# Kernel tuning notes

Measured on AMD Instinct MI355X. Metric: run time of the kernel, lower is better.

Reference implementation:

```python
import jax, jax.numpy as jnp
import numpy as np

N_HEAD = 16
D_MODEL = 1024
D_K = D_MODEL // N_HEAD  # 64
NEG = -1000000000.0


def setup_inputs() -> dict:
    key = jax.random.key(0)
    ks = jax.random.split(key, 7)
    B, L = 4, 2048
    q = jax.random.normal(ks[0], (B, L, D_MODEL), dtype=jnp.float32)
    k = jax.random.normal(ks[1], (B, L, D_MODEL), dtype=jnp.float32)
    v = jax.random.normal(ks[2], (B, L, D_MODEL), dtype=jnp.float32)
    mask = jnp.ones((B, L, L), dtype=jnp.int32)
    s = 1.0 / np.sqrt(D_MODEL)
    w_q = jax.random.normal(ks[3], (D_MODEL, D_MODEL), dtype=jnp.float32) * s
    w_k = jax.random.normal(ks[4], (D_MODEL, D_MODEL), dtype=jnp.float32) * s
    w_v = jax.random.normal(ks[5], (D_MODEL, D_MODEL), dtype=jnp.float32) * s
    w_o = jax.random.normal(ks[6], (D_MODEL, D_MODEL), dtype=jnp.float32) * s
    return {"q": q, "k": k, "v": v, "w_q": w_q, "w_k": w_k, "w_v": w_v, "w_o": w_o, "mask": mask}


def reference(q, k, v, w_q, w_k, w_v, w_o, mask):
    B, Lq, _ = q.shape
    temperature = jnp.asarray(D_K, q.dtype) ** 0.5
    # Projections (Linear, no bias): x @ W^T, then split heads -> [B, H, L, d_k]
    qh = (q @ w_q.T).reshape(B, Lq, N_HEAD, D_K).transpose(0, 2, 1, 3)
    kh = (k @ w_k.T).reshape(B, -1, N_HEAD, D_K).transpose(0, 2, 1, 3)
    vh = (v @ w_v.T).reshape(B, -1, N_HEAD, D_K).transpose(0, 2, 1, 3)
    # Scaled dot-product attention, full [B, H, Lq, Lk] scores materialized
    attn = jnp.einsum("bhqd,bhkd->bhqk", qh / temperature, kh)
    attn = jnp.where(mask[:, None, :, :] == 0, NEG, attn)
    attn = jax.nn.softmax(attn, axis=-1)  # dropout is identity in eval mode
    out = jnp.einsum("bhqk,bhkd->bhqd", attn, vh)
    out = out.transpose(0, 2, 1, 3).reshape(B, Lq, D_MODEL)
    return out @ w_o.T
```

## Files before the change

### kernel.cpp

```cpp
#include <hip/hip_runtime.h>
#include <stdint.h>

typedef float  f32x4  __attribute__((ext_vector_type(4)));
typedef __bf16 bf16x8 __attribute__((ext_vector_type(8)));
typedef short  s16x8  __attribute__((ext_vector_type(8)));
typedef short  s16x4  __attribute__((ext_vector_type(4)));
typedef unsigned int   u32;
typedef unsigned short u16;
typedef u32 u32x2 __attribute__((ext_vector_type(2)));
typedef u32 u32x4 __attribute__((ext_vector_type(4)));

#define DM 1024
#define LQ 2048
#define NH 16

__device__ __forceinline__ u16 f2bf(float f) {
    unsigned int u = __builtin_bit_cast(unsigned int, f);
    u += 0x7FFFu + ((u >> 16) & 1u);
    return (u16)(u >> 16);
}

__device__ __forceinline__ float fexp2(float x) {
#if __has_builtin(__builtin_amdgcn_exp2f)
    return __builtin_amdgcn_exp2f(x);
#else
    return exp2f(x);
#endif
}

__device__ __forceinline__ u32 cvtpk(float lo, float hi) {
    u32 r;
    asm("v_cvt_pk_bf16_f32 %0, %1, %2" : "=v"(r) : "v"(lo), "v"(hi));
    return r;
}

__device__ __forceinline__ float max3f(float a, float b, float c) {
    float r;
    asm("v_max3_f32 %0, %1, %2, %3" : "=v"(r) : "v"(a), "v"(b), "v"(c));
    return r;
}

__device__ __forceinline__ u32 permb(u32 b, u32 a, u32 sel) {
    u32 r;
    asm("v_perm_b32 %0, %1, %2, %3" : "=v"(r) : "v"(b), "v"(a), "s"(sel));
    return r;
}

__device__ __forceinline__ f32x4 mfma32(s16x8 a, s16x8 b, f32x4 c) {
    return __builtin_amdgcn_mfma_f32_16x16x32_bf16(
        __builtin_bit_cast(bf16x8, a), __builtin_bit_cast(bf16x8, b), c, 0, 0, 0);
}

#define GLD16(gp, lp) __builtin_amdgcn_global_load_lds( \
    (__attribute__((address_space(1))) void*)(gp),      \
    (__attribute__((address_space(3))) void*)(lp), 16, 0, 0)

__global__ void k_cvt_mask(const float4* __restrict__ wq, const float4* __restrict__ wk,
                           const float4* __restrict__ wv, const float4* __restrict__ wo,
                           uint64_t* bwq, uint64_t* bwk, uint64_t* bwv, uint64_t* bwo,
                           const int4* __restrict__ m4, int* flag)
{
    const int NW = 262144;
    const int totw = 4 * NW;
    const int totm = (4 * 2048 * 2048) / 4;
    const int stride = gridDim.x * blockDim.x;
    bool z = false;
    for (int idx = blockIdx.x * blockDim.x + threadIdx.x; idx < totw + totm;
         idx += stride) {
        if (idx < totw) {
            int ji = idx >> 18, off = idx & (NW - 1);
            const float4* s = ji == 0 ? wq : ji == 1 ? wk : ji == 2 ? wv : wo;
            uint64_t* d = ji == 0 ? bwq : ji == 1 ? bwk : ji == 2 ? bwv : bwo;
            float4 f = s[off];
            union { u16 u[4]; uint64_t qq; } rr;
            rr.u[0] = f2bf(f.x); rr.u[1] = f2bf(f.y);
            rr.u[2] = f2bf(f.z); rr.u[3] = f2bf(f.w);
            d[off] = rr.qq;
        } else {
            int4 v = m4[idx - totw];
            if (v.x == 0 || v.y == 0 || v.z == 0 || v.w == 0) z = true;
        }
    }
    if (__ballot(z)) {
        if ((threadIdx.x & 63) == 0) atomicAnd(flag, 0);
    }
}

template <int MODE>
__global__ __launch_bounds__(256) void k_gemm(
    const float* __restrict__ Aq, const float* __restrict__ Ak,
    const float* __restrict__ Av, const u16* __restrict__ Ab,
    const u16* __restrict__ Bw0,
    u16* __restrict__ Cb0, float* __restrict__ Cf, float scale)
{
    constexpr int K = 1024;
    __shared__ char lA[128 * 32 * 2];
    __shared__ char lB[128 * 32 * 2];
    const int t = threadIdx.x, l = t & 63, w = t >> 6;
    const int q = l & 15, g = l >> 4;
    const int z = (MODE == 0) ? blockIdx.z : 0;
    const float* Af = (MODE == 0) ? (z == 0 ? Aq : (z == 1 ? Ak : Av)) : nullptr;
    const u16* Bw = Bw0 + (size_t)z * 1048576;
    u16* Cb = (MODE == 0) ? Cb0 + (size_t)z * 8388608 : nullptr;
    const float scl = (MODE == 0 && z != 0) ? 1.0f : scale;
    const int lin = blockIdx.x;
    const int ytile = ((lin & 7) << 3) | ((lin >> 3) & 7);
    const int xtile = lin >> 6;
    const int m0 = ytile * 128, n0 = xtile * 128;
    const int wr = (w >> 1) * 64, wc = (w & 1) * 64;

    f32x4 acc[4][4];
#pragma unroll
    for (int i = 0; i < 4; i++)
#pragma unroll
        for (int j = 0; j < 4; j++) acc[i][j] = (f32x4){0.f, 0.f, 0.f, 0.f};

    for (int k0 = 0; k0 < K; k0 += 32) {
        if (MODE == 0) {
            float4 f0[2], f1[2];
#pragma unroll
            for (int c = 0; c < 2; c++) {
                int i = c * 256 + t;
                int row = i >> 2, sl = i & 3;
                int ss = sl ^ (row & 3);
                const float* ap = Af + (size_t)(m0 + row) * K + k0 + ss * 8;
                f0[c] = *(const float4*)ap;
                f1[c] = *(const float4*)(ap + 4);
            }
#pragma unroll
            for (int c = 0; c < 2; c++) {
                int i = c * 256 + t;
                int row = i >> 2, sl = i & 3;
                int ss = sl ^ (row & 3);
                GLD16(Bw + (size_t)(n0 + row) * K + k0 + ss * 8, lB + (i - l) * 16);
            }
#pragma unroll
            for (int c = 0; c < 2; c++) {
                int i = c * 256 + t;
                u32x4 pk = {cvtpk(f0[c].x, f0[c].y), cvtpk(f0[c].z, f0[c].w),
                            cvtpk(f1[c].x, f1[c].y), cvtpk(f1[c].z, f1[c].w)};
                *(u32x4*)(lA + i * 16) = pk;
            }
        } else {
#pragma unroll
            for (int c = 0; c < 2; c++) {
                int i = c * 256 + t;
                int row = i >> 2, sl = i & 3;
                int ss = sl ^ (row & 3);
                GLD16(Ab + (size_t)(m0 + row) * K + k0 + ss * 8, lA + (i - l) * 16);
                GLD16(Bw + (size_t)(n0 + row) * K + k0 + ss * 8, lB + (i - l) * 16);
            }
        }
        __syncthreads();
        s16x8 af[4], bfr[4];
#pragma unroll
        for (int mt = 0; mt < 4; mt++) {
            int r = wr + mt * 16 + q;
            af[mt] = *(const s16x8*)(lA + r * 64 + ((g ^ (r & 3)) * 16));
        }
#pragma unroll
        for (int nt = 0; nt < 4; nt++) {
            int r = wc + nt * 16 + q;
            bfr[nt] = *(const s16x8*)(lB + r * 64 + ((g ^ (r & 3)) * 16));
        }
#pragma unroll
        for (int mt = 0; mt < 4; mt++)
#pragma unroll
            for (int nt = 0; nt < 4; nt++)
                acc[mt][nt] = mfma32(bfr[nt], af[mt], acc[mt][nt]);
        __syncthreads();
    }

#pragma unroll
    for (int mt = 0; mt < 4; mt++) {
        int m = m0 + wr + mt * 16 + q;
#pragma unroll
        for (int nt = 0; nt < 4; nt++) {
            int n = n0 + wc + nt * 16 + g * 4;
            f32x4 a = acc[mt][nt];
            if (MODE == 0) {
                int bb = m >> 11, row = m & 2047;
                int h = n >> 6, d = n & 63;
                s16x4 pk;
#pragma unroll
                for (int j = 0; j < 4; j++) pk[j] = (short)f2bf(a[j] * scl);
                *(s16x4*)(Cb + (((size_t)(bb * NH + h) * LQ + row) << 6) + d) = pk;
            } else {
                f32x4 o;
#pragma unroll
                for (int j = 0; j < 4; j++) o[j] = a[j] * scl;
                *(f32x4*)(Cf + (size_t)m * DM + n) = o;
            }
        }
    }
}

__global__ __launch_bounds__(256, 2) void k_attn(
    const u16* __restrict__ Qh, const u16* __restrict__ Kh,
    const u16* __restrict__ Vh, u16* __restrict__ ctx,
    const int* __restrict__ mask, const int* __restrict__ flag)
{
    __shared__ char lds[32768];
    char* lK0 = lds;
    char* lV0 = lds + 16384;
    const int t = threadIdx.x, l = t & 63, w = t >> 6;
    const int g = l >> 4, q = l & 15;
    const int p = blockIdx.x;
    const int bh = (p & 7) * 8 + ((p >> 3) >> 3);
    const int qt = ((p >> 3) & 7) * 256;
    const int allones = *flag;
    const size_t base = (size_t)bh * LQ * 64;
    const int dg = (l & 7) | ((w & 2) << 2);
    const int kg = (l >> 3) | ((w & 1) << 3);

    s16x8 qf[4][2];
#pragma unroll
    for (int qh = 0; qh < 4; qh++)
#pragma unroll
        for (int kh = 0; kh < 2; kh++)
            qf[qh][kh] = *(const s16x8*)(
                Qh + base + (size_t)(qt + w * 64 + qh * 16 + q) * 64 + kh * 32 + g * 8);

    f32x4 oacc[4][4];
#pragma unroll
    for (int qh = 0; qh < 4; qh++)
#pragma unroll
        for (int dt = 0; dt < 4; dt++) oacc[qh][dt] = (f32x4){0.f, 0.f, 0.f, 0.f};
    float mrow[4] = {-1e30f, -1e30f, -1e30f, -1e30f};
    float lrow[4] = {0.f, 0.f, 0.f, 0.f};

    auto stageK = [&](int kt, int b) {
#pragma unroll
        for (int c = 0; c < 2; c++) {
            int i = c * 256 + t;
            int row = i >> 3, sl = i & 7;
            GLD16(Kh + base + (size_t)(kt + row) * 64 + ((sl ^ (row & 7)) * 8),
                  lK0 + b * 8192 + (i - l) * 16);
        }
    };
    auto loadV = [&](int kt, s16x4* vr) {
#pragma unroll
        for (int j = 0; j < 4; j++)
            vr[j] = *(const s16x4*)(Vh + base + (size_t)(kt + kg * 4 + j) * 64 + dg * 4);
    };
    auto writeV = [&](const s16x4* vr, int b) {
        const u32 selLO = 0x05040100u, selHI = 0x07060302u;
        const int u = ((kg & 8) >> 1) | (kg & 3);
        const int bb2 = (kg >> 2) & 1;
        u32x2 vv[4];
#pragma unroll
        for (int j = 0; j < 4; j++) vv[j] = __builtin_bit_cast(u32x2, vr[j]);
#pragma unroll
        for (int jj = 0; jj < 4; jj++) {
            int d = dg * 4 + jj;
            u32 a0 = vv[0][jj >> 1], a1 = vv[1][jj >> 1];
            u32 a2 = vv[2][jj >> 1], a3 = vv[3][jj >> 1];
            u32 sel = (jj & 1) ? selHI : selLO;
            u32x2 pw = {permb(a1, a0, sel), permb(a3, a2, sel)};
            *(s16x4*)(lV0 + b * 8192 + d * 128 + ((u ^ (d & 7)) * 16) + bb2 * 8) =
                __builtin_bit_cast(s16x4, pw);
        }
    };

    {
        s16x4 vr[4];
        stageK(0, 0);
        loadV(0, vr);
        writeV(vr, 0);
    }

    int cur = 0;
    for (int kt = 0; kt < LQ; kt += 64) {
        __syncthreads();
        const bool more = (kt + 64) < LQ;
        s16x4 vr[4];
        if (more) {
            stageK(kt + 64, cur ^ 1);
            loadV(kt + 64, vr);
        }

        f32x4 sc[4][4];
#pragma unroll
        for (int qh = 0; qh < 4; qh++)
#pragma unroll
            for (int ct = 0; ct < 4; ct++) sc[qh][ct] = (f32x4){0.f, 0.f, 0.f, 0.f};
        __builtin_amdgcn_s_setprio(1);
#pragma unroll
        for (int ct = 0; ct < 4; ct++) {
            int kc = ct * 16 + q;
#pragma unroll
            for (int kh = 0; kh < 2; kh++) {
                s16x8 kf = *(const s16x8*)(lK0 + cur * 8192 + kc * 128 +
                                           (((kh * 4 + g) ^ (kc & 7)) * 16));
#pragma unroll
                for (int qh = 0; qh < 4; qh++)
                    sc[qh][ct] = mfma32(kf, qf[qh][kh], sc[qh][ct]);
            }
        }
        __builtin_amdgcn_s_setprio(0);

        if (!allones) {
            int b = bh >> 4;
#pragma unroll
            for (int qh = 0; qh < 4; qh++)
#pragma unroll
                for (int ct = 0; ct < 4; ct++)
#pragma unroll
                    for (int r = 0; r < 4; r++) {
                        int qr = qt + w * 64 + qh * 16 + q;
                        int kc = kt + ct * 16 + g * 4 + r;
                        if (mask[(size_t)(b * LQ + qr) * LQ + kc] == 0)
                            sc[qh][ct][r] = -1e9f;
                    }
        }

        float pm[4];
#pragma unroll
        for (int qh = 0; qh < 4; qh++) {
            float m0 = max3f(sc[qh][0][0], sc[qh][0][1], sc[qh][0][2]);
            m0 = max3f(m0, sc[qh][0][3], sc[qh][1][0]);
            m0 = max3f(m0, sc[qh][1][1], sc[qh][1][2]);
            m0 = max3f(m0, sc[qh][1][3], sc[qh][2][0]);
            m0 = max3f(m0, sc[qh][2][1], sc[qh][2][2]);
            m0 = max3f(m0, sc[qh][2][3], sc[qh][3][0]);
            m0 = max3f(m0, sc[qh][3][1], sc[qh][3][2]);
            m0 = fmaxf(m0, sc[qh][3][3]);
            m0 = fmaxf(m0, __shfl_xor(m0, 16, 64));
            m0 = fmaxf(m0, __shfl_xor(m0, 32, 64));
            pm[qh] = m0;
        }
        bool ok = pm[0] <= mrow[0] + 8.f;
        ok = ok && (pm[1] <= mrow[1] + 8.f);
        ok = ok && (pm[2] <= mrow[2] + 8.f);
        ok = ok && (pm[3] <= mrow[3] + 8.f);
        if (!__all(ok)) {
#pragma unroll
            for (int qh = 0; qh < 4; qh++) {
                float nm = fmaxf(mrow[qh], pm[qh]);
                float corr = fexp2(mrow[qh] - nm);
                mrow[qh] = nm;
                lrow[qh] *= corr;
                float cv[4];
#pragma unroll
                for (int r = 0; r < 4; r++) cv[r] = __shfl(corr, g * 4 + r, 64);
#pragma unroll
                for (int dt = 0; dt < 4; dt++)
#pragma unroll
                    for (int r = 0; r < 4; r++) oacc[qh][dt][r] *= cv[r];
            }
        }
        s16x8 pa32[4][2];
#pragma unroll
        for (int qh = 0; qh < 4; qh++) {
#pragma unroll
            for (int ct = 0; ct < 4; ct++)
#pragma unroll
                for (int r = 0; r < 4; r++)
                    sc[qh][ct][r] = fexp2(sc[qh][ct][r] - mrow[qh]);
            f32x4 vs = (sc[qh][0] + sc[qh][1]) + (sc[qh][2] + sc[qh][3]);
            float rs = (vs[0] + vs[1]) + (vs[2] + vs[3]);
            rs += __shfl_xor(rs, 16, 64);
            rs += __shfl_xor(rs, 32, 64);
            lrow[qh] += rs;
#pragma unroll
            for (int s = 0; s < 2; s++) {
                u32x4 pv;
                pv.x = cvtpk(sc[qh][2 * s][0],     sc[qh][2 * s][1]);
                pv.y = cvtpk(sc[qh][2 * s][2],     sc[qh][2 * s][3]);
                pv.z = cvtpk(sc[qh][2 * s + 1][0], sc[qh][2 * s + 1][1]);
                pv.w = cvtpk(sc[qh][2 * s + 1][2], sc[qh][2 * s + 1][3]);
                pa32[qh][s] = __builtin_bit_cast(s16x8, pv);
            }
        }

        __builtin_amdgcn_s_setprio(1);
#pragma unroll
        for (int dt = 0; dt < 4; dt++) {
#pragma unroll
            for (int s = 0; s < 2; s++) {
                s16x8 vf = *(const s16x8*)(lV0 + cur * 8192 + (dt * 16 + q) * 128 +
                                           (((4 * s + g) ^ (q & 7)) * 16));
#pragma unroll
                for (int qh = 0; qh < 4; qh++)
                    oacc[qh][dt] = mfma32(pa32[qh][s], vf, oacc[qh][dt]);
            }
        }
        __builtin_amdgcn_s_setprio(0);

        if (more) writeV(vr, cur ^ 1);
        cur ^= 1;
    }

    __syncthreads();
    char* eb = lds + w * 8192;
#pragma unroll
    for (int qh = 0; qh < 4; qh++) {
        float lv[4];
#pragma unroll
        for (int r = 0; r < 4; r++) lv[r] = 1.f / __shfl(lrow[qh], g * 4 + r, 64);
#pragma unroll
        for (int dt = 0; dt < 4; dt++)
#pragma unroll
            for (int r = 0; r < 4; r++) {
                int row = qh * 16 + g * 4 + r;
                int cb = ((dt * 16 + q) * 2) ^ ((row & 7) << 4);
                *(u16*)(eb + row * 128 + cb) = f2bf(oacc[qh][dt][r] * lv[r]);
            }
    }
    __syncthreads();
    const int b = bh >> 4, h = bh & 15;
    const int token = qt + w * 64 + l;
    u16* gp = ctx + (size_t)(b * LQ + token) * DM + h * 64;
#pragma unroll
    for (int j = 0; j < 8; j++) {
        int cb = (j * 16) ^ ((l & 7) << 4);
        *(s16x8*)(gp + j * 8) = *(const s16x8*)(eb + l * 128 + cb);
    }
}

extern "C" void kernel_launch(void* const* d_in, const int* in_sizes, int n_in,
                              void* d_out, int out_size, void* d_ws, size_t ws_size,
                              hipStream_t stream)
{
    const float* q  = (const float*)d_in[0];
    const float* k  = (const float*)d_in[1];
    const float* v  = (const float*)d_in[2];
    const float* wq = (const float*)d_in[3];
    const float* wk = (const float*)d_in[4];
    const float* wv = (const float*)d_in[5];
    const float* wo = (const float*)d_in[6];
    const int* mask = (const int*)d_in[7];

    char* ws = (char*)d_ws;
    const size_t SX = (size_t)8192 * 1024 * 2;
    const size_t SW = (size_t)1024 * 1024 * 2;
    u16* bwq = (u16*)(ws + 3 * SX);
    u16* bwk = (u16*)(ws + 3 * SX + SW);
    u16* bwv = (u16*)(ws + 3 * SX + 2 * SW);
    u16* bwo = (u16*)(ws + 3 * SX + 3 * SW);
    u16* Qh  = (u16*)(ws + 3 * SX + 4 * SW);
    u16* Kh  = (u16*)(ws + 4 * SX + 4 * SW);
    u16* Vh  = (u16*)(ws + 5 * SX + 4 * SW);
    u16* ctx = (u16*)(ws + 6 * SX + 4 * SW);
    int* flag = (int*)(ws + 7 * SX + 4 * SW);

    hipMemsetAsync(flag, 0xFF, 4, stream);
    k_cvt_mask<<<2048, 256, 0, stream>>>(
        (const float4*)wq, (const float4*)wk, (const float4*)wv, (const float4*)wo,
        (uint64_t*)bwq, (uint64_t*)bwk, (uint64_t*)bwv, (uint64_t*)bwo,
        (const int4*)mask, flag);

    k_gemm<0><<<dim3(512, 1, 3), 256, 0, stream>>>(
        q, k, v, nullptr, bwq, Qh, nullptr, 0.18033688011112042f);

    k_attn<<<512, 256, 0, stream>>>(Qh, Kh, Vh, ctx, mask, flag);

    k_gemm<1><<<dim3(512), 256, 0, stream>>>(
        nullptr, nullptr, nullptr, ctx, bwo, nullptr, (float*)d_out, 1.0f);
}
```

Baseline: 239.7 us.

## Pre-convert activations to bf16 and double-buffer GEMM LDS loads

Adds a separate kernel that converts the q, k and v activations to bf16 in workspace, so the projection GEMM can load A through global_load_lds like the output GEMM. The GEMM now double-buffers its LDS tiles, prefetching the next K-slice during the MFMAs, drops one barrier per iteration, and raises wave priority around the MFMA block. This targets load latency and conversion work inside the GEMM main loop. The cost is an extra pass that reads 96MB of fp32 and writes 48MB of bf16, plus doubled LDS per block.

```diff
diff --git a/kernel.cpp b/kernel.cpp
--- a/kernel.cpp
+++ b/kernel.cpp
@@ -54,6 +54,25 @@
 #define GLD16(gp, lp) __builtin_amdgcn_global_load_lds( \
     (__attribute__((address_space(1))) void*)(gp),      \
     (__attribute__((address_space(3))) void*)(lp), 16, 0, 0)
+
+__global__ void k_cvt_act(const float4* __restrict__ q, const float4* __restrict__ k,
+                          const float4* __restrict__ v,
+                          uint64_t* xq, uint64_t* xk, uint64_t* xv)
+{
+    const int NX = 2097152;
+    const int stride = gridDim.x * blockDim.x;
+    for (int idx = blockIdx.x * blockDim.x + threadIdx.x; idx < 3 * NX;
+         idx += stride) {
+        int ji = idx >> 21, off = idx & (NX - 1);
+        const float4* s = ji == 0 ? q : ji == 1 ? k : v;
+        uint64_t* d = ji == 0 ? xq : ji == 1 ? xk : xv;
+        float4 f = s[off];
+        union { u16 u[4]; uint64_t qq; } rr;
+        rr.u[0] = f2bf(f.x); rr.u[1] = f2bf(f.y);
+        rr.u[2] = f2bf(f.z); rr.u[3] = f2bf(f.w);
+        d[off] = rr.qq;
+    }
+}
 
 __global__ void k_cvt_mask(const float4* __restrict__ wq, const float4* __restrict__ wk,
                            const float4* __restrict__ wv, const float4* __restrict__ wo,
@@ -88,18 +107,16 @@
 
 template <int MODE>
 __global__ __launch_bounds__(256) void k_gemm(
-    const float* __restrict__ Aq, const float* __restrict__ Ak,
-    const float* __restrict__ Av, const u16* __restrict__ Ab,
-    const u16* __restrict__ Bw0,
+    const u16* __restrict__ A0, const u16* __restrict__ Bw0,
     u16* __restrict__ Cb0, float* __restrict__ Cf, float scale)
 {
     constexpr int K = 1024;
-    __shared__ char lA[128 * 32 * 2];
-    __shared__ char lB[128 * 32 * 2];
+    __shared__ char lA[2][8192];
+    __shared__ char lB[2][8192];
     const int t = threadIdx.x, l = t & 63, w = t >> 6;
     const int q = l & 15, g = l >> 4;
     const int z = (MODE == 0) ? blockIdx.z : 0;
-    const float* Af = (MODE == 0) ? (z == 0 ? Aq : (z == 1 ? Ak : Av)) : nullptr;
+    const u16* A  = A0  + (size_t)z * 8388608;
     const u16* Bw = Bw0 + (size_t)z * 1048576;
     u16* Cb = (MODE == 0) ? Cb0 + (size_t)z * 8388608 : nullptr;
     const float scl = (MODE == 0 && z != 0) ? 1.0f : scale;
@@ -115,60 +132,41 @@
 #pragma unroll
         for (int j = 0; j < 4; j++) acc[i][j] = (f32x4){0.f, 0.f, 0.f, 0.f};
 
+    auto stage = [&](int k0, int b) {
+#pragma unroll
+        for (int c = 0; c < 2; c++) {
+            int i = c * 256 + t;
+            int row = i >> 2, sl = i & 3;
+            int ss = sl ^ (row & 3);
+            GLD16(A  + (size_t)(m0 + row) * K + k0 + ss * 8, lA[b] + (i - l) * 16);
+            GLD16(Bw + (size_t)(n0 + row) * K + k0 + ss * 8, lB[b] + (i - l) * 16);
+        }
+    };
+
+    stage(0, 0);
+    int cur = 0;
     for (int k0 = 0; k0 < K; k0 += 32) {
-        if (MODE == 0) {
-            float4 f0[2], f1[2];
-#pragma unroll
-            for (int c = 0; c < 2; c++) {
-                int i = c * 256 + t;
-                int row = i >> 2, sl = i & 3;
-                int ss = sl ^ (row & 3);
-                const float* ap = Af + (size_t)(m0 + row) * K + k0 + ss * 8;
-                f0[c] = *(const float4*)ap;
-                f1[c] = *(const float4*)(ap + 4);
-            }
-#pragma unroll
-            for (int c = 0; c < 2; c++) {
-                int i = c * 256 + t;
-                int row = i >> 2, sl = i & 3;
-                int ss = sl ^ (row & 3);
-                GLD16(Bw + (size_t)(n0 + row) * K + k0 + ss * 8, lB + (i - l) * 16);
-            }
-#pragma unroll
-            for (int c = 0; c < 2; c++) {
-                int i = c * 256 + t;
-                u32x4 pk = {cvtpk(f0[c].x, f0[c].y), cvtpk(f0[c].z, f0[c].w),
-                            cvtpk(f1[c].x, f1[c].y), cvtpk(f1[c].z, f1[c].w)};
-                *(u32x4*)(lA + i * 16) = pk;
-            }
-        } else {
-#pragma unroll
-            for (int c = 0; c < 2; c++) {
-                int i = c * 256 + t;
-                int row = i >> 2, sl = i & 3;
-                int ss = sl ^ (row & 3);
-                GLD16(Ab + (size_t)(m0 + row) * K + k0 + ss * 8, lA + (i - l) * 16);
-                GLD16(Bw + (size_t)(n0 + row) * K + k0 + ss * 8, lB + (i - l) * 16);
-            }
-        }
         __syncthreads();
+        if (k0 + 32 < K) stage(k0 + 32, cur ^ 1);
         s16x8 af[4], bfr[4];
 #pragma unroll
         for (int mt = 0; mt < 4; mt++) {
             int r = wr + mt * 16 + q;
-            af[mt] = *(const s16x8*)(lA + r * 64 + ((g ^ (r & 3)) * 16));
+            af[mt] = *(const s16x8*)(lA[cur] + r * 64 + ((g ^ (r & 3)) * 16));
         }
 #pragma unroll
         for (int nt = 0; nt < 4; nt++) {
             int r = wc + nt * 16 + q;
-            bfr[nt] = *(const s16x8*)(lB + r * 64 + ((g ^ (r & 3)) * 16));
-        }
+            bfr[nt] = *(const s16x8*)(lB[cur] + r * 64 + ((g ^ (r & 3)) * 16));
+        }
+        __builtin_amdgcn_s_setprio(1);
 #pragma unroll
         for (int mt = 0; mt < 4; mt++)
 #pragma unroll
             for (int nt = 0; nt < 4; nt++)
                 acc[mt][nt] = mfma32(bfr[nt], af[mt], acc[mt][nt]);
-        __syncthreads();
+        __builtin_amdgcn_s_setprio(0);
+        cur ^= 1;
     }
 
 #pragma unroll
@@ -434,6 +432,9 @@
     char* ws = (char*)d_ws;
     const size_t SX = (size_t)8192 * 1024 * 2;
     const size_t SW = (size_t)1024 * 1024 * 2;
+    u16* xq  = (u16*)(ws);
+    u16* xk  = (u16*)(ws + SX);
+    u16* xv  = (u16*)(ws + 2 * SX);
     u16* bwq = (u16*)(ws + 3 * SX);
     u16* bwk = (u16*)(ws + 3 * SX + SW);
     u16* bwv = (u16*)(ws + 3 * SX + 2 * SW);
@@ -445,16 +446,18 @@
     int* flag = (int*)(ws + 7 * SX + 4 * SW);
 
     hipMemsetAsync(flag, 0xFF, 4, stream);
+    k_cvt_act<<<2048, 256, 0, stream>>>((const float4*)q, (const float4*)k,
+                                        (const float4*)v,
+                                        (uint64_t*)xq, (uint64_t*)xk, (uint64_t*)xv);
     k_cvt_mask<<<2048, 256, 0, stream>>>(
         (const float4*)wq, (const float4*)wk, (const float4*)wv, (const float4*)wo,
         (uint64_t*)bwq, (uint64_t*)bwk, (uint64_t*)bwv, (uint64_t*)bwo,
         (const int4*)mask, flag);
 
-    k_gemm<0><<<dim3(512, 1, 3), 256, 0, stream>>>(
-        q, k, v, nullptr, bwq, Qh, nullptr, 0.18033688011112042f);
+    k_gemm<0><<<dim3(512, 1, 3), 256, 0, stream>>>(xq, bwq, Qh, nullptr,
+                                                   0.18033688011112042f);
 
     k_attn<<<512, 256, 0, stream>>>(Qh, Kh, Vh, ctx, mask, flag);
 
-    k_gemm<1><<<dim3(512), 256, 0, stream>>>(
-        nullptr, nullptr, nullptr, ctx, bwo, nullptr, (float*)d_out, 1.0f);
-}
+    k_gemm<1><<<dim3(512), 256, 0, stream>>>(ctx, bwo, nullptr, (float*)d_out, 1.0f);
+}
```

After: 253.4 us. 1.06x slower.
